# Kernel optimization log

Hardware: AMD Instinct MI355X
Metric: run time of the kernel (lower is better)

## Reference

```python
import jax, jax.numpy as jnp
import numpy as np

WS = 7   # window_size
SS = 3   # shift_size
NH = 6   # num_heads
EPS = 1e-5


def _partition(x, ws):
    # [b,h,w,c] -> [b*(h//ws)*(w//ws), ws*ws, c]
    b, h, w, c = x.shape
    x = x.reshape(b, h // ws, ws, w // ws, ws, c)
    return x.transpose(0, 1, 3, 2, 4, 5).reshape(-1, ws * ws, c)


def _reverse(windows, ws, h, w, b):
    c = windows.shape[-1]
    x = windows.reshape(b, h // ws, w // ws, ws, ws, c)
    return x.transpose(0, 1, 3, 2, 4, 5).reshape(b, h, w, c)


def _make_mask(h, w, ws, ss):
    # static (numpy) shifted-window attention mask, [nw, ws*ws, ws*ws]
    img = np.zeros((h, w), dtype=np.float32)
    slices = (slice(0, -ws), slice(-ws, -ss), slice(-ss, None))
    cnt = 0
    for hs in slices:
        for wsl in slices:
            img[hs, wsl] = cnt
            cnt += 1
    mw = img.reshape(h // ws, ws, w // ws, ws).transpose(0, 2, 1, 3).reshape(-1, ws * ws)
    am = mw[:, None, :] - mw[:, :, None]
    mask = np.where(am != 0, -100.0, 0.0).astype(np.float32)
    return jnp.asarray(mask)


def _layernorm(x, g, b):
    mu = jnp.mean(x, axis=-1, keepdims=True)
    var = jnp.var(x, axis=-1, keepdims=True)
    return (x - mu) * jax.lax.rsqrt(var + EPS) * g + b


def setup_inputs() -> dict:
    key = jax.random.key(0)
    ks = jax.random.split(key, 8)
    dim = 192
    s = lambda fan: 1.0 / np.sqrt(fan)
    return {
        "x": jax.random.normal(ks[0], (64, 56, 56, dim), dtype=jnp.float32),
        "n1_g": jnp.ones((dim,), jnp.float32),
        "n1_b": jnp.zeros((dim,), jnp.float32),
        "qkv_w": jax.random.normal(ks[1], (dim, 3 * dim), jnp.float32) * s(dim),
        "qkv_b": jnp.zeros((3 * dim,), jnp.float32),
        "proj_w": jax.random.normal(ks[2], (dim, dim), jnp.float32) * s(dim),
        "proj_b": jnp.zeros((dim,), jnp.float32),
        "n2_g": jnp.ones((dim,), jnp.float32),
        "n2_b": jnp.zeros((dim,), jnp.float32),
        "w1": jax.random.normal(ks[3], (dim, 4 * dim), jnp.float32) * s(dim),
        "b1": jnp.zeros((4 * dim,), jnp.float32),
        "w2": jax.random.normal(ks[4], (4 * dim, dim), jnp.float32) * s(4 * dim),
        "b2": jnp.zeros((dim,), jnp.float32),
    }


def reference(x, n1_g, n1_b, qkv_w, qkv_b, proj_w, proj_b, n2_g, n2_b, w1, b1, w2, b2):
    b, h, w, c = x.shape
    hd = c // NH
    scale = hd ** -0.5

    sc = x
    xn = _layernorm(x, n1_g, n1_b)
    sx = jnp.roll(xn, shift=(-SS, -SS), axis=(1, 2))

    xw = _partition(sx, WS)                      # [B_, n, c], n = WS*WS
    B_, n, _ = xw.shape

    qkv = xw @ qkv_w + qkv_b                      # [B_, n, 3c]
    qkv = qkv.reshape(B_, n, 3, NH, hd).transpose(2, 0, 3, 1, 4)
    q, k, v = qkv[0], qkv[1], qkv[2]              # [B_, NH, n, hd]

    attn = jnp.einsum("whnd,whmd->whnm", q, k) * scale   # [B_, NH, n, n]
    mask = _make_mask(h, w, WS, SS)               # [nw, n, n]
    nw = mask.shape[0]
    attn = attn.reshape(b // nw * 1 if False else b, nw, NH, n, n) if False else attn.reshape(B_ // nw, nw, NH, n, n)
    attn = attn + mask[None, :, None, :, :]
    attn = attn.reshape(-1, NH, n, n)
    attn = jax.nn.softmax(attn, axis=-1)

    out = jnp.einsum("whnm,whmd->whnd", attn, v)  # [B_, NH, n, hd]
    out = out.transpose(0, 2, 1, 3).reshape(B_, n, c)
    out = out @ proj_w + proj_b

    sx = _reverse(out, WS, h, w, b)
    xs = jnp.roll(sx, shift=(SS, SS), axis=(1, 2))

    x2 = sc + xs
    x2n = _layernorm(x2, n2_g, n2_b)
    mlp = jax.nn.gelu(x2n @ w1 + b1, approximate=False) @ w2 + b2
    return x2 + mlp
```

## Files before the change

kernel.cpp:

```cpp
#include <hip/hip_runtime.h>

typedef __attribute__((ext_vector_type(4))) float f32x4;
typedef __attribute__((ext_vector_type(8))) short bf16x8;
typedef __attribute__((ext_vector_type(2))) unsigned int u32x2;

#define NHEAD 6

__device__ __forceinline__ unsigned short f2bf(float f){
  union{float f;unsigned int u;}c; c.f=f;
  unsigned int x=c.u;
  return (unsigned short)((x + 0x7FFFu + ((x>>16)&1u)) >> 16);
}
__device__ __forceinline__ unsigned int cvtpk(float a, float b){
  unsigned int r;
  asm("v_cvt_pk_bf16_f32 %0, %1, %2" : "=v"(r) : "v"(a), "v"(b));
  return r;
}

__global__ void wt_kernel(const float* __restrict__ w, unsigned short* __restrict__ wt,
                          int K, int N){
  int idx = blockIdx.x*256 + threadIdx.x;
  if (idx >= K*N) return;
  int k = idx / N, n = idx - k*N;
  wt[(size_t)n*K + k] = f2bf(w[idx]);
}

__global__ __launch_bounds__(256) void ln_kernel(const float* __restrict__ x,
    const float* __restrict__ gw, const float* __restrict__ bw,
    unsigned short* __restrict__ out){
  int tok  = blockIdx.x*4 + (threadIdx.x>>6);
  int lane = threadIdx.x & 63;
  const float* row = x + (size_t)tok*192;
  float4 v = make_float4(0.f,0.f,0.f,0.f);
  if (lane < 48) v = *(const float4*)(row + lane*4);
  float s  = v.x+v.y+v.z+v.w;
  float s2 = v.x*v.x+v.y*v.y+v.z*v.z+v.w*v.w;
  #pragma unroll
  for (int off=32; off; off>>=1){ s += __shfl_xor(s,off); s2 += __shfl_xor(s2,off); }
  float mu = s*(1.f/192.f);
  float rs = rsqrtf(s2*(1.f/192.f) - mu*mu + 1e-5f);
  int b = tok/3136; int hw = tok - b*3136; int h = hw/56; int w = hw - h*56;
  int hs = h-3; if (hs<0) hs += 56;
  int wsh = w-3; if (wsh<0) wsh += 56;
  int wr = hs/7, r = hs - wr*7, wc = wsh/7, c = wsh - wc*7;
  size_t otok = ((size_t)b*64 + wr*8 + wc)*49 + r*7 + c;
  if (lane < 48){
    int cb = lane*4;
    float4 g4 = *(const float4*)(gw + cb);
    float4 b4 = *(const float4*)(bw + cb);
    u32x2 o;
    o.x = cvtpk((v.x-mu)*rs*g4.x + b4.x, (v.y-mu)*rs*g4.y + b4.y);
    o.y = cvtpk((v.z-mu)*rs*g4.z + b4.z, (v.w-mu)*rs*g4.w + b4.w);
    *(u32x2*)(out + otok*192 + cb) = o;
  }
}

__device__ __forceinline__ float gelu_fast(float v){
  float t = v*(1.59576912f + 0.07135481f*v*v);
  float e = __expf(-t);
  return v/(1.f + e);
}

__device__ __forceinline__ size_t proj_rowbase(int grow){
  int winr = grow/49; int nn = grow - winr*49;
  int b  = winr>>6; int wi = winr&63; int wr_ = wi>>3; int wc_ = wi&7;
  int r7 = nn/7;  int c7 = nn - r7*7;
  int h = wr_*7 + r7 + 3; if (h>=56) h-=56;
  int w = wc_*7 + c7 + 3; if (w>=56) w-=56;
  return (((size_t)b*3136) + h*56 + w)*192;
}

__global__ __launch_bounds__(512) void gemm_qkv(
    const unsigned short* __restrict__ A,
    const unsigned short* __restrict__ BT,
    const float* __restrict__ bias,
    unsigned short* __restrict__ Cout,
    int Nb, int K)
{
  __shared__ unsigned short lA[256*64];
  __shared__ unsigned short lB[64*64];
  const int tid  = threadIdx.x;
  const int wave = tid>>6, lane = tid&63;
  const int wm = wave>>1, wn = wave&1;
  const int lr = lane&15, lh = lane>>4;

  int bid = blockIdx.x;
  int yb = bid/(8*Nb); int rr = bid - yb*8*Nb; int xq = rr>>3; int y8 = rr&7;
  const int m0 = (yb*8 + y8)*256, n0 = xq*64;

  f32x4 zero = {0.f,0.f,0.f,0.f};
  f32x4 acc[4][2];
  #pragma unroll
  for (int i=0;i<4;i++){ acc[i][0]=zero; acc[i][1]=zero; }

  const int row8 = tid>>3;
  const int csw  = ((tid&7) ^ (row8&7))*8;
  const unsigned short* Ag = A  + (size_t)(m0 + row8)*K + csw;
  const unsigned short* Bg = BT + (size_t)(n0 + row8)*K + csw;

  for (int kt=0; kt<K; kt+=64){
    __syncthreads();
    #pragma unroll
    for (int i=0;i<4;i++){
      __builtin_amdgcn_global_load_lds(
        (const __attribute__((address_space(1))) void*)(Ag + (size_t)i*64*K + kt),
        (__attribute__((address_space(3))) void*)(lA + i*4096 + wave*512),
        16, 0, 0);
    }
    __builtin_amdgcn_global_load_lds(
      (const __attribute__((address_space(1))) void*)(Bg + kt),
      (__attribute__((address_space(3))) void*)(lB + wave*512),
      16, 0, 0);
    __syncthreads();

    bf16x8 af[4][2], bfv[2][2];
    #pragma unroll
    for (int mi=0;mi<4;mi++)
      #pragma unroll
      for (int ks=0;ks<2;ks++){
        int arow = wm*64+mi*16+lr;
        af[mi][ks] = *(const bf16x8*)&lA[arow*64 + (((ks*4+lh) ^ (lr&7))*8)];
      }
    #pragma unroll
    for (int ni=0;ni<2;ni++)
      #pragma unroll
      for (int ks=0;ks<2;ks++){
        int brow = wn*32+ni*16+lr;
        bfv[ni][ks] = *(const bf16x8*)&lB[brow*64 + (((ks*4+lh) ^ (lr&7))*8)];
      }
    #pragma unroll
    for (int mi=0;mi<4;mi++)
      #pragma unroll
      for (int ni=0;ni<2;ni++)
        #pragma unroll
        for (int ks=0;ks<2;ks++)
          acc[mi][ni] = __builtin_amdgcn_mfma_f32_16x16x32_bf16(
              bfv[ni][ks], af[mi][ks], acc[mi][ni], 0,0,0);
  }

  #pragma unroll
  for (int mi=0;mi<4;mi++){
    const int row = m0 + wm*64 + mi*16 + lr;
    int winr = row/49; int nn = row - winr*49;
    #pragma unroll
    for (int ni=0;ni<2;ni++){
      const int colb = n0 + wn*32 + ni*16 + lh*4;
      float4 bv4 = *(const float4*)(bias + colb);
      int which = colb/192; int rem = colb - which*192;
      int head = rem>>5, d = rem&31;
      size_t idx = (size_t)winr*28224 + (size_t)which*9408 + head*1568 + nn*32 + d;
      u32x2 st;
      st.x = cvtpk(acc[mi][ni][0]+bv4.x, acc[mi][ni][1]+bv4.y);
      st.y = cvtpk(acc[mi][ni][2]+bv4.z, acc[mi][ni][3]+bv4.w);
      *(u32x2*)(Cout + idx) = st;
    }
  }
}

__global__ __launch_bounds__(512) void proj_ln(
    const unsigned short* __restrict__ A,
    const unsigned short* __restrict__ BT,
    const float* __restrict__ bias,
    const float* __restrict__ xres,
    const float* __restrict__ g2, const float* __restrict__ b2n,
    float* __restrict__ x2, unsigned short* __restrict__ x2n)
{
  __shared__ unsigned short lA[256*64];
  __shared__ unsigned short lB[192*64];
  __shared__ float lred[256*4];
  const int tid  = threadIdx.x;
  const int wave = tid>>6, lane = tid&63;
  const int wm = wave>>1, wn = wave&1;
  const int lr = lane&15, lh = lane>>4;
  const int m0 = blockIdx.x*256;
  const int K = 192;

  f32x4 zero = {0.f,0.f,0.f,0.f};
  f32x4 acc[4][6];
  #pragma unroll
  for (int i=0;i<4;i++)
    #pragma unroll
    for (int j=0;j<6;j++) acc[i][j]=zero;

  const int row8 = tid>>3;
  const int csw  = ((tid&7) ^ (row8&7))*8;
  const unsigned short* Ag = A + (size_t)(m0 + row8)*K + csw;

  for (int kt=0; kt<K; kt+=64){
    __syncthreads();
    #pragma unroll
    for (int i=0;i<4;i++){
      __builtin_amdgcn_global_load_lds(
        (const __attribute__((address_space(1))) void*)(Ag + (size_t)i*64*K + kt),
        (__attribute__((address_space(3))) void*)(lA + i*4096 + wave*512),
        16, 0, 0);
    }
    #pragma unroll
    for (int p=0;p<3;p++){
      __builtin_amdgcn_global_load_lds(
        (const __attribute__((address_space(1))) void*)(BT + (size_t)(p*64+row8)*K + kt + csw),
        (__attribute__((address_space(3))) void*)(lB + p*4096 + wave*512),
        16, 0, 0);
    }
    __syncthreads();

    bf16x8 af[4][2], bfv[6][2];
    #pragma unroll
    for (int mi=0;mi<4;mi++)
      #pragma unroll
      for (int ks=0;ks<2;ks++){
        int arow = wm*64+mi*16+lr;
        af[mi][ks] = *(const bf16x8*)&lA[arow*64 + (((ks*4+lh) ^ (lr&7))*8)];
      }
    #pragma unroll
    for (int ni=0;ni<6;ni++)
      #pragma unroll
      for (int ks=0;ks<2;ks++){
        int brow = wn*96+ni*16+lr;
        bfv[ni][ks] = *(const bf16x8*)&lB[brow*64 + (((ks*4+lh) ^ (lr&7))*8)];
      }
    #pragma unroll
    for (int mi=0;mi<4;mi++)
      #pragma unroll
      for (int ni=0;ni<6;ni++)
        #pragma unroll
        for (int ks=0;ks<2;ks++)
          acc[mi][ni] = __builtin_amdgcn_mfma_f32_16x16x32_bf16(
              bfv[ni][ks], af[mi][ks], acc[mi][ni], 0,0,0);
  }

  size_t prows[4];
  #pragma unroll
  for (int mi=0;mi<4;mi++){
    const int grow = m0 + wm*64 + mi*16 + lr;
    size_t pr = proj_rowbase(grow);
    prows[mi] = pr;
    float ss = 0.f, ss2 = 0.f;
    #pragma unroll
    for (int ni=0;ni<6;ni++){
      const int col = wn*96 + ni*16 + lh*4;
      float4 bv4 = *(const float4*)(bias + col);
      float4 rv  = *(const float4*)(xres + pr + col);
      f32x4 v;
      v[0] = acc[mi][ni][0] + bv4.x + rv.x;
      v[1] = acc[mi][ni][1] + bv4.y + rv.y;
      v[2] = acc[mi][ni][2] + bv4.z + rv.z;
      v[3] = acc[mi][ni][3] + bv4.w + rv.w;
      *(float4*)(x2 + pr + col) = make_float4(v[0],v[1],v[2],v[3]);
      acc[mi][ni] = v;
      ss  += v[0]+v[1]+v[2]+v[3];
      ss2 += v[0]*v[0]+v[1]*v[1]+v[2]*v[2]+v[3]*v[3];
    }
    ss  += __shfl_xor(ss,16);  ss2 += __shfl_xor(ss2,16);
    ss  += __shfl_xor(ss,32);  ss2 += __shfl_xor(ss2,32);
    int lrow = wm*64 + mi*16 + lr;
    lred[lrow*4 + wn*2 + 0] = ss;
    lred[lrow*4 + wn*2 + 1] = ss2;
  }
  __syncthreads();
  #pragma unroll
  for (int mi=0;mi<4;mi++){
    int lrow = wm*64 + mi*16 + lr;
    float S  = lred[lrow*4+0] + lred[lrow*4+2];
    float S2 = lred[lrow*4+1] + lred[lrow*4+3];
    float mu = S*(1.f/192.f);
    float rs = rsqrtf(S2*(1.f/192.f) - mu*mu + 1e-5f);
    size_t pr = prows[mi];
    #pragma unroll
    for (int ni=0;ni<6;ni++){
      const int col = wn*96 + ni*16 + lh*4;
      float4 g4 = *(const float4*)(g2 + col);
      float4 b4 = *(const float4*)(b2n + col);
      f32x4 v = acc[mi][ni];
      u32x2 st;
      st.x = cvtpk((v[0]-mu)*rs*g4.x + b4.x, (v[1]-mu)*rs*g4.y + b4.y);
      st.y = cvtpk((v[2]-mu)*rs*g4.z + b4.z, (v[3]-mu)*rs*g4.w + b4.w);
      *(u32x2*)(x2n + pr + col) = st;
    }
  }
}

__global__ __launch_bounds__(512) void mlp_fused(
    const unsigned short* __restrict__ A,
    const unsigned short* __restrict__ W1T,
    const float* __restrict__ b1,
    const unsigned short* __restrict__ W2T,
    const float* __restrict__ b2,
    const float* __restrict__ res,
    float* __restrict__ out)
{
  __shared__ unsigned short lA[256*64];
  __shared__ unsigned short lB1[64*64];
  __shared__ unsigned short lB2[192*64];
  const int tid  = threadIdx.x;
  const int wave = tid>>6, lane = tid&63;
  const int wm = wave>>1, wn = wave&1;
  const int lr = lane&15, lh = lane>>4;
  const int m0 = blockIdx.x*256;

  f32x4 zero = {0.f,0.f,0.f,0.f};
  f32x4 oacc[4][6];
  #pragma unroll
  for (int i=0;i<4;i++)
    #pragma unroll
    for (int j=0;j<6;j++) oacc[i][j]=zero;

  const int row8 = tid>>3;
  const int csw  = ((tid&7) ^ (row8&7))*8;
  const unsigned short* Ag = A + (size_t)(m0 + row8)*192 + csw;

  for (int c=0; c<12; ++c){
    f32x4 hacc[4][2];
    #pragma unroll
    for (int i=0;i<4;i++){ hacc[i][0]=zero; hacc[i][1]=zero; }

    __syncthreads();
    #pragma unroll
    for (int p=0;p<3;p++){
      __builtin_amdgcn_global_load_lds(
        (const __attribute__((address_space(1))) void*)(W2T + (size_t)(p*64+row8)*768 + c*64 + csw),
        (__attribute__((address_space(3))) void*)(lB2 + p*4096 + wave*512),
        16, 0, 0);
    }
    #pragma unroll
    for (int ks1=0; ks1<3; ++ks1){
      if (ks1) __syncthreads();
      #pragma unroll
      for (int i=0;i<4;i++){
        __builtin_amdgcn_global_load_lds(
          (const __attribute__((address_space(1))) void*)(Ag + (size_t)i*64*192 + ks1*64),
          (__attribute__((address_space(3))) void*)(lA + i*4096 + wave*512),
          16, 0, 0);
      }
      __builtin_amdgcn_global_load_lds(
        (const __attribute__((address_space(1))) void*)(W1T + (size_t)(c*64+row8)*192 + ks1*64 + csw),
        (__attribute__((address_space(3))) void*)(lB1 + wave*512),
        16, 0, 0);
      __syncthreads();

      bf16x8 af[4][2], bf1[2][2];
      #pragma unroll
      for (int mi=0;mi<4;mi++)
        #pragma unroll
        for (int ks=0;ks<2;ks++){
          int arow = wm*64+mi*16+lr;
          af[mi][ks] = *(const bf16x8*)&lA[arow*64 + (((ks*4+lh) ^ (lr&7))*8)];
        }
      #pragma unroll
      for (int ni=0;ni<2;ni++)
        #pragma unroll
        for (int ks=0;ks<2;ks++){
          int brow = wn*32+ni*16+lr;
          bf1[ni][ks] = *(const bf16x8*)&lB1[brow*64 + (((ks*4+lh) ^ (lr&7))*8)];
        }
      #pragma unroll
      for (int mi=0;mi<4;mi++)
        #pragma unroll
        for (int ni=0;ni<2;ni++)
          #pragma unroll
          for (int ks=0;ks<2;ks++)
            hacc[mi][ni] = __builtin_amdgcn_mfma_f32_16x16x32_bf16(
                bf1[ni][ks], af[mi][ks], hacc[mi][ni], 0,0,0);
    }
    __syncthreads();
    #pragma unroll
    for (int mi=0;mi<4;mi++){
      int row = wm*64 + mi*16 + lr;
      #pragma unroll
      for (int ni=0;ni<2;ni++){
        int n1 = c*64 + wn*32 + ni*16 + lh*4;
        float4 bb = *(const float4*)(b1 + n1);
        u32x2 st;
        st.x = cvtpk(gelu_fast(hacc[mi][ni][0]+bb.x), gelu_fast(hacc[mi][ni][1]+bb.y));
        st.y = cvtpk(gelu_fast(hacc[mi][ni][2]+bb.z), gelu_fast(hacc[mi][ni][3]+bb.w));
        int c16 = wn*4 + ni*2 + (lh>>1);
        int byte = row*128 + ((c16 ^ (row&7))*16) + (lh&1)*8;
        *(u32x2*)((char*)lA + byte) = st;
      }
    }
    __syncthreads();
    #pragma unroll
    for (int ks2=0; ks2<2; ++ks2){
      bf16x8 afh[4], bf2[6];
      #pragma unroll
      for (int mi=0;mi<4;mi++){
        int arow = wm*64+mi*16+lr;
        afh[mi] = *(const bf16x8*)&lA[arow*64 + (((ks2*4+lh) ^ (lr&7))*8)];
      }
      #pragma unroll
      for (int ni=0;ni<6;ni++){
        int brow = wn*96+ni*16+lr;
        bf2[ni] = *(const bf16x8*)&lB2[brow*64 + (((ks2*4+lh) ^ (lr&7))*8)];
      }
      #pragma unroll
      for (int mi=0;mi<4;mi++)
        #pragma unroll
        for (int ni=0;ni<6;ni++)
          oacc[mi][ni] = __builtin_amdgcn_mfma_f32_16x16x32_bf16(
              bf2[ni], afh[mi], oacc[mi][ni], 0,0,0);
    }
  }

  #pragma unroll
  for (int mi=0;mi<4;mi++){
    const int grow = m0 + wm*64 + mi*16 + lr;
    #pragma unroll
    for (int ni=0;ni<6;ni++){
      const int col = wn*96 + ni*16 + lh*4;
      size_t idx = (size_t)grow*192 + col;
      float4 bb = *(const float4*)(b2 + col);
      float4 rv = *(const float4*)(res + idx);
      *(float4*)(out + idx) = make_float4(
          rv.x + oacc[mi][ni][0] + bb.x,
          rv.y + oacc[mi][ni][1] + bb.y,
          rv.z + oacc[mi][ni][2] + bb.z,
          rv.w + oacc[mi][ni][3] + bb.w);
    }
  }
}

__global__ __launch_bounds__(256) void attn_kernel(const unsigned short* __restrict__ qkv,
                                                   unsigned short* __restrict__ aout){
  __shared__ __align__(16) unsigned short ldsQK[4][4096];
  __shared__ __align__(16) unsigned short ldsV[4][2048];
  const int wave = threadIdx.x>>6, lane = threadIdx.x&63;
  const int lr = lane&15, lh = lane>>4;
  const int unit = blockIdx.x*4 + wave;
  const int win  = unit/NHEAD, head = unit - win*NHEAD;

  unsigned short* Q  = ldsQK[wave];
  unsigned short* Kl = ldsQK[wave] + 2048;
  unsigned short* P  = ldsQK[wave];
  unsigned short* Vt = ldsV[wave];

  const size_t wbase = (size_t)win*28224 + (size_t)head*1568;
  const unsigned short* gQ = qkv + wbase;
  const unsigned short* gK = qkv + wbase + 9408;
  const unsigned short* gV = qkv + wbase + 18816;

  {
    uint4 z = make_uint4(0,0,0,0);
    #pragma unroll
    for (int i=0;i<4;i++) *(uint4*)&Vt[(i*64+lane)*8] = z;
  }

  #pragma unroll
  for (int i=0;i<4;i++){
    int idx = i*64 + lane;
    if (idx < 196){
      int row = idx>>2, blk = idx&3;
      int sb = (blk ^ (row&3) ^ ((row>>2)&3));
      uint4 dq = *(const uint4*)(gQ + idx*8);
      *(uint4*)&Q[row*32 + sb*8] = dq;
      uint4 dk = *(const uint4*)(gK + idx*8);
      *(uint4*)&Kl[row*32 + sb*8] = dk;
    }
  }
  #pragma unroll
  for (int i=0;i<4;i++){
    int idx = i*64 + lane;
    if (idx < 196){
      int row = idx>>2, d0 = (idx&3)*8;
      uint4 dv = *(const uint4*)(gV + idx*8);
      unsigned int wds[4] = {dv.x, dv.y, dv.z, dv.w};
      int rb = row>>3, re = row&7;
      #pragma unroll
      for (int j=0;j<8;j++){
        unsigned short t = (unsigned short)(wds[j>>1] >> ((j&1)*16));
        Vt[(d0+j)*64 + ((rb ^ j)*8) + re] = t;
      }
    }
  }

  bf16x8 kf[4], qf[4];
  #pragma unroll
  for (int t=0;t<4;t++){
    int row = t*16 + lr;
    int off = row*32 + ((lh ^ (row&3) ^ ((row>>2)&3))*8);
    kf[t] = *(const bf16x8*)&Kl[off];
    qf[t] = *(const bf16x8*)&Q[off];
  }

  f32x4 zero = {0.f,0.f,0.f,0.f};
  f32x4 S[4][4];
  #pragma unroll
  for (int mi=0;mi<4;mi++)
    #pragma unroll
    for (int ni=0;ni<4;ni++)
      S[mi][ni] = __builtin_amdgcn_mfma_f32_16x16x32_bf16(kf[mi], qf[ni], zero, 0,0,0);

  const int wi = win & 63, wr = wi>>3, wc = wi&7;
  const bool hasmask = (wr==7) || (wc==7);
  const float scale = 0.17677669529663687f;

  #pragma unroll
  for (int ni=0;ni<4;ni++){
    int q = ni*16 + lr;
    int idq = 0;
    if (hasmask){
      int qr = q/7, qc = q - qr*7;
      int ih = (wr==7) ? ((qr>=4)?2:1) : 0;
      int iw = (wc==7) ? ((qc>=4)?2:1) : 0;
      idq = ih*3 + iw;
    }
    #pragma unroll
    for (int mi=0;mi<4;mi++){
      #pragma unroll
      for (int r=0;r<4;r++){
        int key = mi*16 + lh*4 + r;
        float s;
        if (key >= 49) s = -1e30f;
        else {
          float add = 0.f;
          if (hasmask){
            int kr = key/7, kc = key - kr*7;
            int ih = (wr==7) ? ((kr>=4)?2:1) : 0;
            int iw = (wc==7) ? ((kc>=4)?2:1) : 0;
            add = ((ih*3+iw) == idq) ? 0.f : -100.f;
          }
          s = S[mi][ni][r]*scale + add;
        }
        S[mi][ni][r] = s;
      }
    }
    float m = -1e30f;
    #pragma unroll
    for (int mi=0;mi<4;mi++)
      #pragma unroll
      for (int r=0;r<4;r++) m = fmaxf(m, S[mi][ni][r]);
    m = fmaxf(m, __shfl_xor(m, 16));
    m = fmaxf(m, __shfl_xor(m, 32));
    float sum = 0.f;
    #pragma unroll
    for (int mi=0;mi<4;mi++)
      #pragma unroll
      for (int r=0;r<4;r++){
        float p = __expf(S[mi][ni][r] - m);
        S[mi][ni][r] = p; sum += p;
      }
    sum += __shfl_xor(sum, 16);
    sum += __shfl_xor(sum, 32);
    float inv = 1.f/sum;
    #pragma unroll
    for (int mi=0;mi<4;mi++){
      int keyb = mi*16 + lh*4;
      int blk = keyb>>3, e0 = keyb&7;
      int addr = q*64 + ((blk ^ (q&7))*8) + e0;
      *(unsigned int*)&P[addr]   = cvtpk(S[mi][ni][0]*inv, S[mi][ni][1]*inv);
      *(unsigned int*)&P[addr+2] = cvtpk(S[mi][ni][2]*inv, S[mi][ni][3]*inv);
    }
  }

  bf16x8 vf[2][2];
  #pragma unroll
  for (int mt=0;mt<2;mt++)
    #pragma unroll
    for (int ks=0;ks<2;ks++){
      int row = mt*16 + lr;
      vf[mt][ks] = *(const bf16x8*)&Vt[row*64 + (((ks*4+lh) ^ (row&7))*8)];
    }
  f32x4 O[2][4];
  #pragma unroll
  for (int ni=0;ni<4;ni++){
    int q = ni*16 + lr;
    bf16x8 pf0 = *(const bf16x8*)&P[q*64 + (((0*4+lh) ^ (q&7))*8)];
    bf16x8 pf1 = *(const bf16x8*)&P[q*64 + (((1*4+lh) ^ (q&7))*8)];
    #pragma unroll
    for (int mt=0;mt<2;mt++){
      f32x4 t = __builtin_amdgcn_mfma_f32_16x16x32_bf16(vf[mt][0], pf0, zero, 0,0,0);
      O[mt][ni] = __builtin_amdgcn_mfma_f32_16x16x32_bf16(vf[mt][1], pf1, t, 0,0,0);
    }
  }

  #pragma unroll
  for (int ni=0;ni<4;ni++){
    int q = ni*16 + lr;
    if (q < 49){
      size_t ob = ((size_t)win*49 + q)*192 + head*32 + lh*4;
      #pragma unroll
      for (int mt=0;mt<2;mt++){
        u32x2 st;
        st.x = cvtpk(O[mt][ni][0], O[mt][ni][1]);
        st.y = cvtpk(O[mt][ni][2], O[mt][ni][3]);
        *(u32x2*)(aout + ob + mt*16) = st;
      }
    }
  }
}

extern "C" void kernel_launch(void* const* d_in, const int* in_sizes, int n_in,
                              void* d_out, int out_size, void* d_ws, size_t ws_size,
                              hipStream_t stream){
  (void)in_sizes; (void)n_in; (void)out_size; (void)ws_size;
  const float* x      = (const float*)d_in[0];
  const float* n1_g   = (const float*)d_in[1];
  const float* n1_b   = (const float*)d_in[2];
  const float* qkv_w  = (const float*)d_in[3];
  const float* qkv_b  = (const float*)d_in[4];
  const float* proj_w = (const float*)d_in[5];
  const float* proj_b = (const float*)d_in[6];
  const float* n2_g   = (const float*)d_in[7];
  const float* n2_b   = (const float*)d_in[8];
  const float* w1     = (const float*)d_in[9];
  const float* b1     = (const float*)d_in[10];
  const float* w2     = (const float*)d_in[11];
  const float* b2     = (const float*)d_in[12];

  char* ws = (char*)d_ws;
  unsigned short* qkvT = (unsigned short*)(ws + 0);
  unsigned short* projT= (unsigned short*)(ws + 221184);
  unsigned short* w1T  = (unsigned short*)(ws + 294912);
  unsigned short* w2T  = (unsigned short*)(ws + 589824);
  unsigned short* bufA = (unsigned short*)(ws + 884736);
  unsigned short* bufQ = (unsigned short*)(ws + 77955072);
  float*          x2   = (float*)        (ws + 309166080);
  unsigned short* x2n  = (unsigned short*)(ws + 463306752);
  float* out = (float*)d_out;

  wt_kernel<<<432,256,0,stream>>>(qkv_w, qkvT, 192, 576);
  wt_kernel<<<144,256,0,stream>>>(proj_w, projT, 192, 192);
  wt_kernel<<<576,256,0,stream>>>(w1,    w1T,  192, 768);
  wt_kernel<<<576,256,0,stream>>>(w2,    w2T,  768, 192);

  ln_kernel<<<50176,256,0,stream>>>(x, n1_g, n1_b, bufA);
  gemm_qkv<<<9*784, 512,0,stream>>>(bufA, qkvT, qkv_b, bufQ, 9, 192);
  attn_kernel<<<6144,256,0,stream>>>(bufQ, bufA);
  proj_ln<<<784, 512,0,stream>>>(bufA, projT, proj_b, x, n2_g, n2_b, x2, x2n);
  mlp_fused<<<784, 512,0,stream>>>(x2n, w1T, b1, w2T, b2, x2, out);
}
```

Baseline: 830.0 us.

## Split fused MLP into two generic GEMM launches with templated epilogues

Replaces the single fused MLP kernel (which kept the GELU hidden activations in LDS) with a templated GEMM kernel used twice: once for W1 with a bias+GELU epilogue writing bf16 hidden activations to a global buffer, and once for W2 with a bias+residual epilogue staged through LDS for coalesced fp32 stores. This is meant to raise parallelism and drop the serialized per-chunk syncs of the fused kernel. In exchange it adds a large round trip of the hidden activations through global memory.

Result: faster. 758.4 us (-8.6%).

```diff
diff --git a/kernel.cpp b/kernel.cpp
--- a/kernel.cpp
+++ b/kernel.cpp
@@ -55,6 +55,8 @@
   }
 }
 
+enum { EPI_QKV=0, EPI_GELU=2, EPI_FINAL=3 };
+
 __device__ __forceinline__ float gelu_fast(float v){
   float t = v*(1.59576912f + 0.07135481f*v*v);
   float e = __expf(-t);
@@ -70,12 +72,14 @@
   return (((size_t)b*3136) + h*56 + w)*192;
 }
 
-__global__ __launch_bounds__(512) void gemm_qkv(
+template<int EPI>
+__global__ __launch_bounds__(512) void gemm_k(
     const unsigned short* __restrict__ A,
     const unsigned short* __restrict__ BT,
     const float* __restrict__ bias,
-    unsigned short* __restrict__ Cout,
-    int Nb, int K)
+    const float* __restrict__ res,
+    void* __restrict__ Cout,
+    int N, int Nb, int K)
 {
   __shared__ unsigned short lA[256*64];
   __shared__ unsigned short lB[64*64];
@@ -138,21 +142,65 @@
               bfv[ni][ks], af[mi][ks], acc[mi][ni], 0,0,0);
   }
 
-  #pragma unroll
-  for (int mi=0;mi<4;mi++){
-    const int row = m0 + wm*64 + mi*16 + lr;
-    int winr = row/49; int nn = row - winr*49;
-    #pragma unroll
-    for (int ni=0;ni<2;ni++){
-      const int colb = n0 + wn*32 + ni*16 + lh*4;
-      float4 bv4 = *(const float4*)(bias + colb);
-      int which = colb/192; int rem = colb - which*192;
-      int head = rem>>5, d = rem&31;
-      size_t idx = (size_t)winr*28224 + (size_t)which*9408 + head*1568 + nn*32 + d;
-      u32x2 st;
-      st.x = cvtpk(acc[mi][ni][0]+bv4.x, acc[mi][ni][1]+bv4.y);
-      st.y = cvtpk(acc[mi][ni][2]+bv4.z, acc[mi][ni][3]+bv4.w);
-      *(u32x2*)(Cout + idx) = st;
+  if (EPI == EPI_QKV || EPI == EPI_GELU){
+    #pragma unroll
+    for (int mi=0;mi<4;mi++){
+      const int row = m0 + wm*64 + mi*16 + lr;
+      int winr = row/49; int nn = row - winr*49;
+      #pragma unroll
+      for (int ni=0;ni<2;ni++){
+        const int colb = n0 + wn*32 + ni*16 + lh*4;
+        float4 bv4 = *(const float4*)(bias + colb);
+        float v0 = acc[mi][ni][0] + bv4.x;
+        float v1 = acc[mi][ni][1] + bv4.y;
+        float v2 = acc[mi][ni][2] + bv4.z;
+        float v3 = acc[mi][ni][3] + bv4.w;
+        u32x2 st;
+        if (EPI == EPI_GELU){
+          st.x = cvtpk(gelu_fast(v0), gelu_fast(v1));
+          st.y = cvtpk(gelu_fast(v2), gelu_fast(v3));
+          *(u32x2*)((unsigned short*)Cout + (size_t)row*N + colb) = st;
+        } else {
+          int which = colb/192; int rem = colb - which*192;
+          int head = rem>>5, d = rem&31;
+          size_t idx = (size_t)winr*28224 + (size_t)which*9408 + head*1568 + nn*32 + d;
+          st.x = cvtpk(v0,v1); st.y = cvtpk(v2,v3);
+          *(u32x2*)((unsigned short*)Cout + idx) = st;
+        }
+      }
+    }
+  } else {
+    float* Tf = (float*)lA;
+    #pragma unroll
+    for (int h=0; h<2; ++h){
+      __syncthreads();
+      if ((wave>>2) == h){
+        #pragma unroll
+        for (int mi=0;mi<4;mi++){
+          int lrow = (wm&1)*64 + mi*16 + lr;
+          #pragma unroll
+          for (int ni=0;ni<2;ni++){
+            int colb = n0 + wn*32 + ni*16 + lh*4;
+            float4 bv4 = *(const float4*)(bias + colb);
+            float4 val = make_float4(acc[mi][ni][0]+bv4.x, acc[mi][ni][1]+bv4.y,
+                                     acc[mi][ni][2]+bv4.z, acc[mi][ni][3]+bv4.w);
+            int c4 = wn*8 + ni*4 + lh;
+            *(float4*)&Tf[lrow*64 + ((c4 ^ (lrow&15))*4)] = val;
+          }
+        }
+      }
+      __syncthreads();
+      #pragma unroll
+      for (int rnd=0; rnd<4; ++rnd){
+        int lrow = rnd*32 + (tid>>4);
+        int chunk = tid&15;
+        float4 v = *(const float4*)&Tf[lrow*64 + ((chunk ^ (lrow&15))*4)];
+        int grow = m0 + h*128 + lrow;
+        size_t base = (size_t)grow*N + n0 + chunk*4;
+        float4 rv = *(const float4*)(res + base);
+        *(float4*)((float*)Cout + base) =
+            make_float4(rv.x+v.x, rv.y+v.y, rv.z+v.z, rv.w+v.w);
+      }
     }
   }
 }
@@ -280,145 +328,6 @@
   }
 }
 
-__global__ __launch_bounds__(512) void mlp_fused(
-    const unsigned short* __restrict__ A,
-    const unsigned short* __restrict__ W1T,
-    const float* __restrict__ b1,
-    const unsigned short* __restrict__ W2T,
-    const float* __restrict__ b2,
-    const float* __restrict__ res,
-    float* __restrict__ out)
-{
-  __shared__ unsigned short lA[256*64];
-  __shared__ unsigned short lB1[64*64];
-  __shared__ unsigned short lB2[192*64];
-  const int tid  = threadIdx.x;
-  const int wave = tid>>6, lane = tid&63;
-  const int wm = wave>>1, wn = wave&1;
-  const int lr = lane&15, lh = lane>>4;
-  const int m0 = blockIdx.x*256;
-
-  f32x4 zero = {0.f,0.f,0.f,0.f};
-  f32x4 oacc[4][6];
-  #pragma unroll
-  for (int i=0;i<4;i++)
-    #pragma unroll
-    for (int j=0;j<6;j++) oacc[i][j]=zero;
-
-  const int row8 = tid>>3;
-  const int csw  = ((tid&7) ^ (row8&7))*8;
-  const unsigned short* Ag = A + (size_t)(m0 + row8)*192 + csw;
-
-  for (int c=0; c<12; ++c){
-    f32x4 hacc[4][2];
-    #pragma unroll
-    for (int i=0;i<4;i++){ hacc[i][0]=zero; hacc[i][1]=zero; }
-
-    __syncthreads();
-    #pragma unroll
-    for (int p=0;p<3;p++){
-      __builtin_amdgcn_global_load_lds(
-        (const __attribute__((address_space(1))) void*)(W2T + (size_t)(p*64+row8)*768 + c*64 + csw),
-        (__attribute__((address_space(3))) void*)(lB2 + p*4096 + wave*512),
-        16, 0, 0);
-    }
-    #pragma unroll
-    for (int ks1=0; ks1<3; ++ks1){
-      if (ks1) __syncthreads();
-      #pragma unroll
-      for (int i=0;i<4;i++){
-        __builtin_amdgcn_global_load_lds(
-          (const __attribute__((address_space(1))) void*)(Ag + (size_t)i*64*192 + ks1*64),
-          (__attribute__((address_space(3))) void*)(lA + i*4096 + wave*512),
-          16, 0, 0);
-      }
-      __builtin_amdgcn_global_load_lds(
-        (const __attribute__((address_space(1))) void*)(W1T + (size_t)(c*64+row8)*192 + ks1*64 + csw),
-        (__attribute__((address_space(3))) void*)(lB1 + wave*512),
-        16, 0, 0);
-      __syncthreads();
-
-      bf16x8 af[4][2], bf1[2][2];
-      #pragma unroll
-      for (int mi=0;mi<4;mi++)
-        #pragma unroll
-        for (int ks=0;ks<2;ks++){
-          int arow = wm*64+mi*16+lr;
-          af[mi][ks] = *(const bf16x8*)&lA[arow*64 + (((ks*4+lh) ^ (lr&7))*8)];
-        }
-      #pragma unroll
-      for (int ni=0;ni<2;ni++)
-        #pragma unroll
-        for (int ks=0;ks<2;ks++){
-          int brow = wn*32+ni*16+lr;
-          bf1[ni][ks] = *(const bf16x8*)&lB1[brow*64 + (((ks*4+lh) ^ (lr&7))*8)];
-        }
-      #pragma unroll
-      for (int mi=0;mi<4;mi++)
-        #pragma unroll
-        for (int ni=0;ni<2;ni++)
-          #pragma unroll
-          for (int ks=0;ks<2;ks++)
-            hacc[mi][ni] = __builtin_amdgcn_mfma_f32_16x16x32_bf16(
-                bf1[ni][ks], af[mi][ks], hacc[mi][ni], 0,0,0);
-    }
-    __syncthreads();
-    #pragma unroll
-    for (int mi=0;mi<4;mi++){
-      int row = wm*64 + mi*16 + lr;
-      #pragma unroll
-      for (int ni=0;ni<2;ni++){
-        int n1 = c*64 + wn*32 + ni*16 + lh*4;
-        float4 bb = *(const float4*)(b1 + n1);
-        u32x2 st;
-        st.x = cvtpk(gelu_fast(hacc[mi][ni][0]+bb.x), gelu_fast(hacc[mi][ni][1]+bb.y));
-        st.y = cvtpk(gelu_fast(hacc[mi][ni][2]+bb.z), gelu_fast(hacc[mi][ni][3]+bb.w));
-        int c16 = wn*4 + ni*2 + (lh>>1);
-        int byte = row*128 + ((c16 ^ (row&7))*16) + (lh&1)*8;
-        *(u32x2*)((char*)lA + byte) = st;
-      }
-    }
-    __syncthreads();
-    #pragma unroll
-    for (int ks2=0; ks2<2; ++ks2){
-      bf16x8 afh[4], bf2[6];
-      #pragma unroll
-      for (int mi=0;mi<4;mi++){
-        int arow = wm*64+mi*16+lr;
-        afh[mi] = *(const bf16x8*)&lA[arow*64 + (((ks2*4+lh) ^ (lr&7))*8)];
-      }
-      #pragma unroll
-      for (int ni=0;ni<6;ni++){
-        int brow = wn*96+ni*16+lr;
-        bf2[ni] = *(const bf16x8*)&lB2[brow*64 + (((ks2*4+lh) ^ (lr&7))*8)];
-      }
-      #pragma unroll
-      for (int mi=0;mi<4;mi++)
-        #pragma unroll
-        for (int ni=0;ni<6;ni++)
-          oacc[mi][ni] = __builtin_amdgcn_mfma_f32_16x16x32_bf16(
-              bf2[ni], afh[mi], oacc[mi][ni], 0,0,0);
-    }
-  }
-
-  #pragma unroll
-  for (int mi=0;mi<4;mi++){
-    const int grow = m0 + wm*64 + mi*16 + lr;
-    #pragma unroll
-    for (int ni=0;ni<6;ni++){
-      const int col = wn*96 + ni*16 + lh*4;
-      size_t idx = (size_t)grow*192 + col;
-      float4 bb = *(const float4*)(b2 + col);
-      float4 rv = *(const float4*)(res + idx);
-      *(float4*)(out + idx) = make_float4(
-          rv.x + oacc[mi][ni][0] + bb.x,
-          rv.y + oacc[mi][ni][1] + bb.y,
-          rv.z + oacc[mi][ni][2] + bb.z,
-          rv.w + oacc[mi][ni][3] + bb.w);
-    }
-  }
-}
-
 __global__ __launch_bounds__(256) void attn_kernel(const unsigned short* __restrict__ qkv,
                                                    unsigned short* __restrict__ aout){
   __shared__ __align__(16) unsigned short ldsQK[4][4096];
@@ -613,6 +522,7 @@
   unsigned short* w2T  = (unsigned short*)(ws + 589824);
   unsigned short* bufA = (unsigned short*)(ws + 884736);
   unsigned short* bufQ = (unsigned short*)(ws + 77955072);
+  unsigned short* hbuf = (unsigned short*)(ws + 884736);
   float*          x2   = (float*)        (ws + 309166080);
   unsigned short* x2n  = (unsigned short*)(ws + 463306752);
   float* out = (float*)d_out;
@@ -623,8 +533,9 @@
   wt_kernel<<<576,256,0,stream>>>(w2,    w2T,  768, 192);
 
   ln_kernel<<<50176,256,0,stream>>>(x, n1_g, n1_b, bufA);
-  gemm_qkv<<<9*784, 512,0,stream>>>(bufA, qkvT, qkv_b, bufQ, 9, 192);
+  gemm_k<EPI_QKV  ><<< 9*784, 512,0,stream>>>(bufA, qkvT, qkv_b, nullptr, bufQ, 576, 9, 192);
   attn_kernel<<<6144,256,0,stream>>>(bufQ, bufA);
   proj_ln<<<784, 512,0,stream>>>(bufA, projT, proj_b, x, n2_g, n2_b, x2, x2n);
-  mlp_fused<<<784, 512,0,stream>>>(x2n, w1T, b1, w2T, b2, x2, out);
-}
+  gemm_k<EPI_GELU ><<<12*784, 512,0,stream>>>(x2n, w1T, b1, nullptr, hbuf, 768, 12, 192);
+  gemm_k<EPI_FINAL><<< 3*784, 512,0,stream>>>(hbuf, w2T, b2, x2, out, 192, 3, 768);
+}
```
